# Performance work log

Hardware: AMD Instinct MI355X
Metric: run time of the kernel (lower is better)

The kernel has to match this reference:

```python
import jax, jax.numpy as jnp
import numpy as np


def setup_inputs() -> dict:
    key = jax.random.key(0)
    k1, k2, k3 = jax.random.split(key, 3)
    B, C, H, W = 64, 512, 32, 32
    l = jax.random.normal(k1, (B, C, H, W), dtype=jnp.float32)
    g = jax.random.normal(k2, (B, C), dtype=jnp.float32)
    # 1x1 Conv2d(C -> 1, bias=False) weight, flattened from [1, C, 1, 1] to [C]
    w = jax.random.normal(k3, (C,), dtype=jnp.float32) * (1.0 / np.sqrt(C))
    return {"l": l, "g": g, "w": w}


def reference(l, g, w):
    B, C, H, W = l.shape
    # broadcast add of global vector, then 1x1 conv == channel dot-product
    x = l + g[:, :, None, None]                      # [B, C, H, W]
    c = jnp.einsum('bchw,c->bhw', x, w)              # [B, H, W]
    # softmax over the flattened spatial dims
    a = jax.nn.softmax(c.reshape(B, -1), axis=1).reshape(B, 1, H, W)
    # attention-weighted spatial pooling of l -> [B, C]
    g_out = jnp.einsum('bchw,bzhw->bc', l, a)
    return (c[:, None, :, :], g_out)
```

## Files before the change

### kernel.cpp

```cpp
#include <hip/hip_runtime.h>

#define B_  64
#define C_  512
#define HW_ 1024
#define NCHUNK 16
#define CPC (C_ / NCHUNK)

__device__ __forceinline__ float waveReduceSum(float v) {
    #pragma unroll
    for (int off = 32; off > 0; off >>= 1) v += __shfl_xor(v, off);
    return v;
}

__device__ __forceinline__ float waveReduceMax(float v) {
    #pragma unroll
    for (int off = 32; off > 0; off >>= 1) v = fmaxf(v, __shfl_xor(v, off));
    return v;
}

__global__ __launch_bounds__(256) void kA_partial_dot(
        const float* __restrict__ l,
        const float* __restrict__ w,
        float* __restrict__ part) {
    const int blk   = blockIdx.x;
    const int b     = blk / NCHUNK;
    const int chunk = blk % NCHUNK;
    const int tid   = threadIdx.x;

    const float4* l4 = reinterpret_cast<const float4*>(
        l + ((size_t)b * C_ + (size_t)chunk * CPC) * HW_);

    float4 acc = {0.f, 0.f, 0.f, 0.f};
    #pragma unroll 8
    for (int i = 0; i < CPC; ++i) {
        const float wv = w[chunk * CPC + i];
        const float4 v = l4[(size_t)i * (HW_ / 4) + tid];
        acc.x = fmaf(v.x, wv, acc.x);
        acc.y = fmaf(v.y, wv, acc.y);
        acc.z = fmaf(v.z, wv, acc.z);
        acc.w = fmaf(v.w, wv, acc.w);
    }
    reinterpret_cast<float4*>(part)[(size_t)blk * (HW_ / 4) + tid] = acc;
}

__global__ __launch_bounds__(256) void kB_softmax_pool(
        const float* __restrict__ l,
        const float* __restrict__ part,
        const float* __restrict__ g,
        const float* __restrict__ w,
        float* __restrict__ c_out,
        float* __restrict__ gout) {
    __shared__ float a_lds[HW_];
    __shared__ float red[4];

    const int blk   = blockIdx.x;
    const int b     = blk >> 4;
    const int chunk = blk & 15;
    const int tid   = threadIdx.x;
    const int lane  = tid & 63;
    const int wid   = tid >> 6;

    float p = g[b * C_ + tid] * w[tid] + g[b * C_ + 256 + tid] * w[256 + tid];
    p = waveReduceSum(p);
    if (lane == 0) red[wid] = p;
    __syncthreads();
    const float gw = red[0] + red[1] + red[2] + red[3];

    const float4* part4 = reinterpret_cast<const float4*>(part);
    float4 c4 = {gw, gw, gw, gw};
    #pragma unroll
    for (int k = 0; k < NCHUNK; ++k) {
        const float4 v = part4[(size_t)(b * NCHUNK + k) * (HW_ / 4) + tid];
        c4.x += v.x; c4.y += v.y; c4.z += v.z; c4.w += v.w;
    }

    float m = fmaxf(fmaxf(c4.x, c4.y), fmaxf(c4.z, c4.w));
    m = waveReduceMax(m);
    __syncthreads();
    if (lane == 0) red[wid] = m;
    __syncthreads();
    m = fmaxf(fmaxf(red[0], red[1]), fmaxf(red[2], red[3]));

    float4 e4;
    e4.x = __expf(c4.x - m);
    e4.y = __expf(c4.y - m);
    e4.z = __expf(c4.z - m);
    e4.w = __expf(c4.w - m);
    float s = e4.x + e4.y + e4.z + e4.w;
    s = waveReduceSum(s);
    __syncthreads();
    if (lane == 0) red[wid] = s;
    __syncthreads();
    s = red[0] + red[1] + red[2] + red[3];
    const float inv = __frcp_rn(s);

    float4 a4 = {e4.x * inv, e4.y * inv, e4.z * inv, e4.w * inv};
    reinterpret_cast<float4*>(a_lds)[tid] = a4;
    if (chunk == 0)
        reinterpret_cast<float4*>(c_out + (size_t)b * HW_)[tid] = c4;
    __syncthreads();

    float4 av[4];
    #pragma unroll
    for (int i = 0; i < 4; ++i)
        av[i] = reinterpret_cast<float4*>(a_lds)[i * 64 + lane];

    #pragma unroll
    for (int ch = 0; ch < 8; ++ch) {
        const int c = chunk * CPC + wid * 8 + ch;
        const float4* l4 = reinterpret_cast<const float4*>(
            l + ((size_t)b * C_ + c) * HW_);
        float sacc = 0.f;
        #pragma unroll
        for (int i = 0; i < 4; ++i) {
            const float4 v = l4[i * 64 + lane];
            sacc = fmaf(v.x, av[i].x, sacc);
            sacc = fmaf(v.y, av[i].y, sacc);
            sacc = fmaf(v.z, av[i].z, sacc);
            sacc = fmaf(v.w, av[i].w, sacc);
        }
        sacc = waveReduceSum(sacc);
        if (lane == 0) gout[(size_t)b * C_ + c] = sacc;
    }
}

extern "C" void kernel_launch(void* const* d_in, const int* in_sizes, int n_in,
                              void* d_out, int out_size, void* d_ws, size_t ws_size,
                              hipStream_t stream) {
    const float* l = (const float*)d_in[0];
    const float* g = (const float*)d_in[1];
    const float* w = (const float*)d_in[2];
    float* out = (float*)d_out;

    float* part = (float*)d_ws;

    kA_partial_dot<<<B_ * NCHUNK, 256, 0, stream>>>(l, w, part);
    kB_softmax_pool<<<B_ * NCHUNK, 256, 0, stream>>>(
        l, part, g, w, out, out + (size_t)B_ * HW_);
}
```

Baseline: 217.6 us.

## Fuse dot and softmax-pool kernels into one cooperative kernel with grid sync

Merges the two launches into a single cooperative kernel that computes the partial channel dot products, does a grid-wide barrier, then runs softmax and pooling. Each block reads the same chunk of l in both phases, so the second read may hit in the last-level cache rather than HBM. The blockIdx mapping is swizzled across 8 groups, apparently to spread work across XCDs, and the g·w term is folded into the partial sums. This relies on all 1024 blocks being co-resident for the cooperative launch and adds the cost of a grid barrier.

```diff
diff --git a/kernel.cpp b/kernel.cpp
--- a/kernel.cpp
+++ b/kernel.cpp
@@ -1,4 +1,7 @@
 #include <hip/hip_runtime.h>
+#include <hip/hip_cooperative_groups.h>
+
+namespace cg = cooperative_groups;
 
 #define B_  64
 #define C_  512
@@ -18,65 +21,55 @@
     return v;
 }
 
-__global__ __launch_bounds__(256) void kA_partial_dot(
+__global__ __launch_bounds__(256, 4) void fused_attn(
         const float* __restrict__ l,
+        const float* __restrict__ g,
         const float* __restrict__ w,
-        float* __restrict__ part) {
-    const int blk   = blockIdx.x;
-    const int b     = blk / NCHUNK;
-    const int chunk = blk % NCHUNK;
+        float* __restrict__ part,
+        float* __restrict__ c_out,
+        float* __restrict__ gout) {
+    __shared__ float a_lds[HW_];
+    __shared__ float red[4];
+
+    const int wg = blockIdx.x;
+    const int id = (wg & 7) * (1024 / 8) + (wg >> 3);
+    const int b     = id >> 4;
+    const int chunk = id & 15;
     const int tid   = threadIdx.x;
+    const int lane  = tid & 63;
+    const int wid   = tid >> 6;
 
-    const float4* l4 = reinterpret_cast<const float4*>(
-        l + ((size_t)b * C_ + (size_t)chunk * CPC) * HW_);
-
+    const float4* l4 = reinterpret_cast<const float4*>(l) +
+                       (size_t)id * CPC * (HW_ / 4);
     float4 acc = {0.f, 0.f, 0.f, 0.f};
+    float gwc = 0.f;
     #pragma unroll 8
     for (int i = 0; i < CPC; ++i) {
-        const float wv = w[chunk * CPC + i];
-        const float4 v = l4[(size_t)i * (HW_ / 4) + tid];
+        const int c = chunk * CPC + i;
+        const float wv = w[c];
+        gwc = fmaf(g[b * C_ + c], wv, gwc);
+        const float4 v = l4[i * (HW_ / 4) + tid];
         acc.x = fmaf(v.x, wv, acc.x);
         acc.y = fmaf(v.y, wv, acc.y);
         acc.z = fmaf(v.z, wv, acc.z);
         acc.w = fmaf(v.w, wv, acc.w);
     }
-    reinterpret_cast<float4*>(part)[(size_t)blk * (HW_ / 4) + tid] = acc;
-}
+    acc.x += gwc; acc.y += gwc; acc.z += gwc; acc.w += gwc;
+    reinterpret_cast<float4*>(part)[(size_t)id * (HW_ / 4) + tid] = acc;
 
-__global__ __launch_bounds__(256) void kB_softmax_pool(
-        const float* __restrict__ l,
-        const float* __restrict__ part,
-        const float* __restrict__ g,
-        const float* __restrict__ w,
-        float* __restrict__ c_out,
-        float* __restrict__ gout) {
-    __shared__ float a_lds[HW_];
-    __shared__ float red[4];
+    cg::this_grid().sync();
 
-    const int blk   = blockIdx.x;
-    const int b     = blk >> 4;
-    const int chunk = blk & 15;
-    const int tid   = threadIdx.x;
-    const int lane  = tid & 63;
-    const int wid   = tid >> 6;
-
-    float p = g[b * C_ + tid] * w[tid] + g[b * C_ + 256 + tid] * w[256 + tid];
-    p = waveReduceSum(p);
-    if (lane == 0) red[wid] = p;
-    __syncthreads();
-    const float gw = red[0] + red[1] + red[2] + red[3];
-
-    const float4* part4 = reinterpret_cast<const float4*>(part);
-    float4 c4 = {gw, gw, gw, gw};
+    const float4* part4 = reinterpret_cast<const float4*>(part) +
+                          (size_t)b * NCHUNK * (HW_ / 4);
+    float4 c4 = {0.f, 0.f, 0.f, 0.f};
     #pragma unroll
     for (int k = 0; k < NCHUNK; ++k) {
-        const float4 v = part4[(size_t)(b * NCHUNK + k) * (HW_ / 4) + tid];
+        const float4 v = part4[k * (HW_ / 4) + tid];
         c4.x += v.x; c4.y += v.y; c4.z += v.z; c4.w += v.w;
     }
 
     float m = fmaxf(fmaxf(c4.x, c4.y), fmaxf(c4.z, c4.w));
     m = waveReduceMax(m);
-    __syncthreads();
     if (lane == 0) red[wid] = m;
     __syncthreads();
     m = fmaxf(fmaxf(red[0], red[1]), fmaxf(red[2], red[3]));
@@ -108,12 +101,12 @@
     #pragma unroll
     for (int ch = 0; ch < 8; ++ch) {
         const int c = chunk * CPC + wid * 8 + ch;
-        const float4* l4 = reinterpret_cast<const float4*>(
-            l + ((size_t)b * C_ + c) * HW_);
+        const float4* lr = reinterpret_cast<const float4*>(l) +
+                           ((size_t)b * C_ + c) * (HW_ / 4);
         float sacc = 0.f;
         #pragma unroll
         for (int i = 0; i < 4; ++i) {
-            const float4 v = l4[i * 64 + lane];
+            const float4 v = lr[i * 64 + lane];
             sacc = fmaf(v.x, av[i].x, sacc);
             sacc = fmaf(v.y, av[i].y, sacc);
             sacc = fmaf(v.z, av[i].z, sacc);
@@ -130,11 +123,13 @@
     const float* l = (const float*)d_in[0];
     const float* g = (const float*)d_in[1];
     const float* w = (const float*)d_in[2];
-    float* out = (float*)d_out;
+    float* c_out = (float*)d_out;
+    float* gout  = (float*)d_out + (size_t)B_ * HW_;
+    float* part  = (float*)d_ws;
 
-    float* part = (float*)d_ws;
-
-    kA_partial_dot<<<B_ * NCHUNK, 256, 0, stream>>>(l, w, part);
-    kB_softmax_pool<<<B_ * NCHUNK, 256, 0, stream>>>(
-        l, part, g, w, out, out + (size_t)B_ * HW_);
+    void* args[] = {(void*)&l, (void*)&g, (void*)&w,
+                    (void*)&part, (void*)&c_out, (void*)&gout};
+    (void)hipLaunchCooperativeKernel((const void*)fused_attn,
+                                     dim3(B_ * NCHUNK), dim3(256),
+                                     args, 0, stream);
 }
```

New measurement: 335.1 us. 1.54x slower.

## Double chunk count, swizzle blocks across XCDs, and batch loads for memory parallelism

Applied to the files above, without the earlier changes.

Splits each batch into 32 channel chunks instead of 16, so both kernels launch twice as many blocks. A block-id swizzle spreads neighbouring ids across the XCDs. The partial-dot kernel issues all of its loads before accumulating, and the pooling kernel interleaves four channel accumulators and batches its partial-sum reads to keep more memory requests in flight. In exchange, the softmax recomputation per block is duplicated more often and the partial-sum workspace doubles in size.

```diff
diff --git a/kernel.cpp b/kernel.cpp
--- a/kernel.cpp
+++ b/kernel.cpp
@@ -3,8 +3,9 @@
 #define B_  64
 #define C_  512
 #define HW_ 1024
-#define NCHUNK 16
+#define NCHUNK 32
 #define CPC (C_ / NCHUNK)
+#define NBLK (B_ * NCHUNK)
 
 __device__ __forceinline__ float waveReduceSum(float v) {
     #pragma unroll
@@ -18,29 +19,35 @@
     return v;
 }
 
+__device__ __forceinline__ int swz(int wg) {
+    return (wg & 7) * (NBLK / 8) + (wg >> 3);
+}
+
 __global__ __launch_bounds__(256) void kA_partial_dot(
         const float* __restrict__ l,
         const float* __restrict__ w,
         float* __restrict__ part) {
-    const int blk   = blockIdx.x;
-    const int b     = blk / NCHUNK;
-    const int chunk = blk % NCHUNK;
-    const int tid   = threadIdx.x;
+    const int id  = swz(blockIdx.x);
+    const int tid = threadIdx.x;
+    const int c0  = (id & (NCHUNK - 1)) * CPC;
 
-    const float4* l4 = reinterpret_cast<const float4*>(
-        l + ((size_t)b * C_ + (size_t)chunk * CPC) * HW_);
+    const float4* l4 = reinterpret_cast<const float4*>(l) +
+                       (size_t)id * CPC * (HW_ / 4);
+
+    float4 v[CPC];
+    #pragma unroll
+    for (int i = 0; i < CPC; ++i) v[i] = l4[i * (HW_ / 4) + tid];
 
     float4 acc = {0.f, 0.f, 0.f, 0.f};
-    #pragma unroll 8
+    #pragma unroll
     for (int i = 0; i < CPC; ++i) {
-        const float wv = w[chunk * CPC + i];
-        const float4 v = l4[(size_t)i * (HW_ / 4) + tid];
-        acc.x = fmaf(v.x, wv, acc.x);
-        acc.y = fmaf(v.y, wv, acc.y);
-        acc.z = fmaf(v.z, wv, acc.z);
-        acc.w = fmaf(v.w, wv, acc.w);
+        const float wv = w[c0 + i];
+        acc.x = fmaf(v[i].x, wv, acc.x);
+        acc.y = fmaf(v[i].y, wv, acc.y);
+        acc.z = fmaf(v[i].z, wv, acc.z);
+        acc.w = fmaf(v[i].w, wv, acc.w);
     }
-    reinterpret_cast<float4*>(part)[(size_t)blk * (HW_ / 4) + tid] = acc;
+    reinterpret_cast<float4*>(part)[(size_t)id * (HW_ / 4) + tid] = acc;
 }
 
 __global__ __launch_bounds__(256) void kB_softmax_pool(
@@ -53,9 +60,9 @@
     __shared__ float a_lds[HW_];
     __shared__ float red[4];
 
-    const int blk   = blockIdx.x;
-    const int b     = blk >> 4;
-    const int chunk = blk & 15;
+    const int id    = swz(blockIdx.x);
+    const int b     = id >> 5;
+    const int chunk = id & (NCHUNK - 1);
     const int tid   = threadIdx.x;
     const int lane  = tid & 63;
     const int wid   = tid >> 6;
@@ -66,12 +73,19 @@
     __syncthreads();
     const float gw = red[0] + red[1] + red[2] + red[3];
 
-    const float4* part4 = reinterpret_cast<const float4*>(part);
+    const float4* part4 = reinterpret_cast<const float4*>(part) +
+                          (size_t)b * NCHUNK * (HW_ / 4);
     float4 c4 = {gw, gw, gw, gw};
     #pragma unroll
-    for (int k = 0; k < NCHUNK; ++k) {
-        const float4 v = part4[(size_t)(b * NCHUNK + k) * (HW_ / 4) + tid];
-        c4.x += v.x; c4.y += v.y; c4.z += v.z; c4.w += v.w;
+    for (int kk = 0; kk < NCHUNK / 8; ++kk) {
+        float4 v[8];
+        #pragma unroll
+        for (int i = 0; i < 8; ++i)
+            v[i] = part4[(kk * 8 + i) * (HW_ / 4) + tid];
+        #pragma unroll
+        for (int i = 0; i < 8; ++i) {
+            c4.x += v[i].x; c4.y += v[i].y; c4.z += v[i].z; c4.w += v[i].w;
+        }
     }
 
     float m = fmaxf(fmaxf(c4.x, c4.y), fmaxf(c4.z, c4.w));
@@ -105,22 +119,25 @@
     for (int i = 0; i < 4; ++i)
         av[i] = reinterpret_cast<float4*>(a_lds)[i * 64 + lane];
 
+    const int cbase = chunk * CPC + wid * 4;
+    const float4* lr = reinterpret_cast<const float4*>(l) +
+                       ((size_t)b * C_ + cbase) * (HW_ / 4);
+    float sacc[4] = {0.f, 0.f, 0.f, 0.f};
     #pragma unroll
-    for (int ch = 0; ch < 8; ++ch) {
-        const int c = chunk * CPC + wid * 8 + ch;
-        const float4* l4 = reinterpret_cast<const float4*>(
-            l + ((size_t)b * C_ + c) * HW_);
-        float sacc = 0.f;
+    for (int i = 0; i < 4; ++i) {
         #pragma unroll
-        for (int i = 0; i < 4; ++i) {
-            const float4 v = l4[i * 64 + lane];
-            sacc = fmaf(v.x, av[i].x, sacc);
-            sacc = fmaf(v.y, av[i].y, sacc);
-            sacc = fmaf(v.z, av[i].z, sacc);
-            sacc = fmaf(v.w, av[i].w, sacc);
+        for (int ch = 0; ch < 4; ++ch) {
+            const float4 v = lr[ch * (HW_ / 4) + i * 64 + lane];
+            sacc[ch] = fmaf(v.x, av[i].x, sacc[ch]);
+            sacc[ch] = fmaf(v.y, av[i].y, sacc[ch]);
+            sacc[ch] = fmaf(v.z, av[i].z, sacc[ch]);
+            sacc[ch] = fmaf(v.w, av[i].w, sacc[ch]);
         }
-        sacc = waveReduceSum(sacc);
-        if (lane == 0) gout[(size_t)b * C_ + c] = sacc;
+    }
+    #pragma unroll
+    for (int ch = 0; ch < 4; ++ch) {
+        const float r = waveReduceSum(sacc[ch]);
+        if (lane == 0) gout[(size_t)b * C_ + cbase + ch] = r;
     }
 }
 
@@ -130,11 +147,10 @@
     const float* l = (const float*)d_in[0];
     const float* g = (const float*)d_in[1];
     const float* w = (const float*)d_in[2];
-    float* out = (float*)d_out;
+    float* c_out = (float*)d_out;
+    float* gout  = (float*)d_out + (size_t)B_ * HW_;
+    float* part  = (float*)d_ws;
 
-    float* part = (float*)d_ws;
-
-    kA_partial_dot<<<B_ * NCHUNK, 256, 0, stream>>>(l, w, part);
-    kB_softmax_pool<<<B_ * NCHUNK, 256, 0, stream>>>(
-        l, part, g, w, out, out + (size_t)B_ * HW_);
+    kA_partial_dot<<<NBLK, 256, 0, stream>>>(l, w, part);
+    kB_softmax_pool<<<NBLK, 256, 0, stream>>>(l, part, g, w, c_out, gout);
 }
```

Measured after the change: 219.6 us. About the same (+0.9%).
